# Kernel optimization log

Measured on AMD Instinct MI355X. Metric: run time of the kernel, lower is better.

## Reference

```python
import jax, jax.numpy as jnp
import numpy as np

N = 30000      # num nodes
E = 600000     # num edges
D = 128        # feature dim (all layers)
R = 7          # num_relation
G = 16         # num graphs in batch
L = 3          # num layers (hidden_dims = [128,128,128])


def setup_inputs() -> dict:
    key = jax.random.key(0)
    ks = jax.random.split(key, 10)
    x = jax.random.normal(ks[0], (N, D), dtype=jnp.float32)
    node_in = jax.random.randint(ks[1], (E,), 0, N)
    node_out = jax.random.randint(ks[2], (E,), 0, N)
    relation = jax.random.randint(ks[3], (E,), 0, R)
    edge_weight = jax.random.uniform(ks[4], (E,), dtype=jnp.float32)
    node2graph = jnp.sort(jax.random.randint(ks[5], (N,), 0, G))
    # learned params: per-layer relational linear (R*D -> D) and self-loop linear (D -> D)
    Wr = jax.random.normal(ks[6], (L, R * D, D), dtype=jnp.float32) * 0.02
    br = jnp.zeros((L, D), dtype=jnp.float32)
    Wl = jax.random.normal(ks[7], (L, D, D), dtype=jnp.float32) * 0.02
    bl = jnp.zeros((L, D), dtype=jnp.float32)
    return dict(x=x, node_in=node_in, node_out=node_out, relation=relation,
                edge_weight=edge_weight, node2graph=node2graph,
                Wr=Wr, br=br, Wl=Wl, bl=bl)


def reference(x, node_in, node_out, relation, edge_weight, node2graph, Wr, br, Wl, bl):
    # relation-indexed destination segment: node_out * R + relation
    seg = node_out * R + relation            # (E,)
    ew = edge_weight[:, None]                # (E, 1)
    h = x
    for i in range(L):
        msg = h[node_in] * ew                                         # gather + weight, (E, D)
        upd = jax.ops.segment_sum(msg, seg, num_segments=N * R)       # scatter_add, (N*R, D)
        upd = upd.reshape(N, R * D)                                   # per-relation concat
        h = jax.nn.relu(upd @ Wr[i] + br[i] + h @ Wl[i] + bl[i])      # linear + self-loop + act
    node_feature = h                                                  # (N, D)
    graph_feature = jax.ops.segment_sum(node_feature, node2graph, num_segments=G)  # sum readout
    return graph_feature, node_feature
```

## Files before the change

kernel.cpp:

```cpp
#include <hip/hip_runtime.h>
#include <hip/hip_bf16.h>

#define NN 30000
#define NE 600000
#define DD 128
#define RR 7
#define GG 16
#define LL 3

#define NB64 ((NN + 63) / 64)

typedef short bf16x8 __attribute__((ext_vector_type(8)));
typedef float f32x4  __attribute__((ext_vector_type(4)));

__device__ __forceinline__ unsigned short f2bf(float f) {
    unsigned u = __float_as_uint(f);
    unsigned r = (u + 0x7fffu + ((u >> 16) & 1u)) >> 16;
    return (unsigned short)r;
}
__device__ __forceinline__ float bf2f(unsigned short b) {
    return __uint_as_float(((unsigned)b) << 16);
}
__device__ __forceinline__ ushort2 pk2bf(float a, float b) {
    __hip_bfloat162 t = __float22bfloat162_rn(make_float2(a, b));
    return *(ushort2*)&t;
}

__device__ __forceinline__ void gl_lds16(const void* g, void* l) {
    __builtin_amdgcn_global_load_lds(
        (const __attribute__((address_space(1))) void*)g,
        (__attribute__((address_space(3))) void*)l, 16, 0, 0);
}

__global__ __launch_bounds__(256) void pack_weights(
    const float* __restrict__ Wl,
    const float* __restrict__ Wr,
    unsigned short* __restrict__ Bw2)
{
    int t = blockIdx.x * 256 + threadIdx.x;
    if (t >= LL * 131072) return;
    int l    = t >> 17;
    int rem  = t & 131071;
    int ch   = rem >> 14;
    int c    = (rem >> 7) & 127;
    int kkin = rem & 127;
    float v;
    if (ch == 0) {
        v = Wl[(size_t)l * 16384 + kkin * 128 + c];
    } else {
        v = Wr[(size_t)l * 114688 + (size_t)((ch - 1) * 128 + kkin) * 128 + c];
    }
    Bw2[t] = f2bf(v);
}

__global__ __launch_bounds__(256) void convert_bf16(
    const float* __restrict__ in, unsigned short* __restrict__ out, int n4)
{
    int i = blockIdx.x * 256 + threadIdx.x;
    if (i >= n4) return;
    float4 v = ((const float4*)in)[i];
    ushort2 lo = pk2bf(v.x, v.y);
    ushort2 hi = pk2bf(v.z, v.w);
    ((ushort4*)out)[i] = make_ushort4(lo.x, lo.y, hi.x, hi.y);
}

__global__ __launch_bounds__(256) void bucket_hist(
    const int* __restrict__ node_out, int* __restrict__ bcnt, int E)
{
    int e = blockIdx.x * 256 + threadIdx.x;
    if (e < E) atomicAdd(&bcnt[(node_out[e] >> 6) * 16], 1);
}

__global__ __launch_bounds__(512) void bucket_scan(
    const int* __restrict__ bcnt, int* __restrict__ bstart,
    int* __restrict__ bcur, int nb)
{
    __shared__ int s[512];
    int t = threadIdx.x;
    int v = (t < nb) ? bcnt[t * 16] : 0;
    s[t] = v;
    __syncthreads();
#pragma unroll
    for (int off = 1; off < 512; off <<= 1) {
        int u = (t >= off) ? s[t - off] : 0;
        __syncthreads();
        s[t] += u;
        __syncthreads();
    }
    if (t <= nb) {
        int excl = s[t] - v;
        bstart[t] = excl;
        if (t < nb) bcur[t * 16] = excl;
    }
}

__global__ __launch_bounds__(256) void bucket_scatter(
    const int* __restrict__ node_in,
    const int* __restrict__ node_out,
    const int* __restrict__ relation,
    const float* __restrict__ ew,
    int* __restrict__ bcur,
    int2* __restrict__ tmp,
    int E)
{
    int e = blockIdx.x * 256 + threadIdx.x;
    if (e >= E) return;
    int o = node_out[e];
    int pos = atomicAdd(&bcur[(o >> 6) * 16], 1);
    tmp[pos] = make_int2(((o & 63) << 18) | (node_in[e] << 3) | relation[e],
                         __float_as_int(ew[e]));
}

__global__ __launch_bounds__(256) void bucket_sort(
    const int2* __restrict__ tmp,
    const int* __restrict__ bstart,
    int2* __restrict__ meta,
    int* __restrict__ start,
    int N)
{
    __shared__ int hist[64];
    __shared__ int scan[64];
    __shared__ int cur[64];
    const int b = blockIdx.x;
    const int t = threadIdx.x;
    const int s0 = bstart[b];
    const int s1 = bstart[b + 1];

    if (t < 64) hist[t] = 0;
    __syncthreads();
    for (int i = s0 + t; i < s1; i += 256)
        atomicAdd(&hist[((unsigned)tmp[i].x) >> 18], 1);
    __syncthreads();

    int v = (t < 64) ? hist[t] : 0;
    if (t < 64) scan[t] = v;
    __syncthreads();
#pragma unroll
    for (int off = 1; off < 64; off <<= 1) {
        int u = (t < 64 && t >= off) ? scan[t - off] : 0;
        __syncthreads();
        if (t < 64) scan[t] += u;
        __syncthreads();
    }
    if (t < 64) {
        int excl = scan[t] - v;
        cur[t] = s0 + excl;
        int node = b * 64 + t;
        if (node <= N) start[node] = s0 + excl;
    }
    __syncthreads();

    for (int i = s0 + t; i < s1; i += 256) {
        int2 m = tmp[i];
        int j = ((unsigned)m.x) >> 18;
        int pos = atomicAdd(&cur[j], 1);
        meta[pos] = make_int2(m.x & 0x3ffff, m.y);
    }
}

__global__ __launch_bounds__(256) void aggregate_h(
    const unsigned short* __restrict__ hb,
    const int* __restrict__ start,
    const int2* __restrict__ meta,
    unsigned short* __restrict__ upd,
    int N)
{
    int wid = (blockIdx.x * 256 + threadIdx.x) >> 6;
    int lane = threadIdx.x & 63;
    if (wid >= N) return;

    int e0 = start[wid];
    int e1 = start[wid + 1];

    float ax[7], ay[7];
#pragma unroll
    for (int r = 0; r < 7; ++r) { ax[r] = 0.f; ay[r] = 0.f; }

#define GATHER(m) (*(const unsigned*)(hb + (((size_t)((m).x >> 3)) << 7) + lane * 2))
#define ACCUM(m, u) do {                                                       \
    float w_  = __int_as_float((m).y);                                         \
    float hx_ = __uint_as_float((u) << 16);                                    \
    float hy_ = __uint_as_float((u) & 0xffff0000u);                            \
    switch (__builtin_amdgcn_readfirstlane((m).x) & 7) {                       \
      case 0: ax[0]=fmaf(w_,hx_,ax[0]); ay[0]=fmaf(w_,hy_,ay[0]); break;       \
      case 1: ax[1]=fmaf(w_,hx_,ax[1]); ay[1]=fmaf(w_,hy_,ay[1]); break;       \
      case 2: ax[2]=fmaf(w_,hx_,ax[2]); ay[2]=fmaf(w_,hy_,ay[2]); break;       \
      case 3: ax[3]=fmaf(w_,hx_,ax[3]); ay[3]=fmaf(w_,hy_,ay[3]); break;       \
      case 4: ax[4]=fmaf(w_,hx_,ax[4]); ay[4]=fmaf(w_,hy_,ay[4]); break;       \
      case 5: ax[5]=fmaf(w_,hx_,ax[5]); ay[5]=fmaf(w_,hy_,ay[5]); break;       \
      default: ax[6]=fmaf(w_,hx_,ax[6]); ay[6]=fmaf(w_,hy_,ay[6]); break;      \
    } } while (0)

    int e = e0;
    for (; e + 4 <= e1; e += 4) {
        int2 m0 = meta[e + 0], m1 = meta[e + 1];
        int2 m2 = meta[e + 2], m3 = meta[e + 3];
        unsigned u0 = GATHER(m0), u1 = GATHER(m1);
        unsigned u2 = GATHER(m2), u3 = GATHER(m3);
        ACCUM(m0, u0); ACCUM(m1, u1); ACCUM(m2, u2); ACCUM(m3, u3);
    }
    for (; e < e1; ++e) {
        int2 m = meta[e];
        unsigned u = GATHER(m);
        ACCUM(m, u);
    }
#undef GATHER
#undef ACCUM

    unsigned short* urow = upd + (size_t)wid * 896 + lane * 2;
#pragma unroll
    for (int r = 0; r < 7; ++r) {
        ushort2 p = pk2bf(ax[r], ay[r]);
        *(unsigned*)(urow + r * 128) = ((unsigned)p.y << 16) | p.x;
    }
}

__global__ __launch_bounds__(256) void gemm_fused(
    const unsigned short* __restrict__ hb,
    const unsigned short* __restrict__ upd,
    const unsigned short* __restrict__ Bw2,
    const float* __restrict__ br,
    const float* __restrict__ bl,
    unsigned short* __restrict__ hout,
    float* __restrict__ nf,
    int N)
{
    __shared__ unsigned short As[64 * 128];
    __shared__ unsigned short Bs[128 * 128];

    const int tid  = threadIdx.x;
    const int wave = tid >> 6;
    const int lane = tid & 63;
    const int quad = lane >> 4;
    const int l16  = lane & 15;
    const int row0 = blockIdx.x * 64;

    const int lr = lane >> 4;
    const int ls = lane & 15;

    f32x4 acc[4][2];
#pragma unroll
    for (int mt = 0; mt < 4; ++mt)
#pragma unroll
        for (int nt = 0; nt < 2; ++nt)
            acc[mt][nt] = (f32x4){0.f, 0.f, 0.f, 0.f};

    const unsigned short* As_l = As + l16 * 128;
    const unsigned short* Bs_l = Bs + (wave * 32 + l16) * 128;
    const int swz = l16 & 7;

    for (int ch = 0; ch < 8; ++ch) {
#pragma unroll
        for (int i = 0; i < 4; ++i) {
            int g = i * 4 + wave;
            int r = g * 4 + lr;
            int slot = ls ^ (r & 7);
            const unsigned short* src;
            if (ch == 0)
                src = hb + (size_t)(row0 + r) * 128 + slot * 8;
            else
                src = upd + (size_t)(row0 + r) * 896 + (ch - 1) * 128 + slot * 8;
            gl_lds16(src, As + g * 512);
        }
        const unsigned short* Bchunk = Bw2 + (size_t)ch * 16384;
#pragma unroll
        for (int i = 0; i < 8; ++i) {
            int g = i * 4 + wave;
            int r = g * 4 + lr;
            int slot = ls ^ (r & 7);
            gl_lds16(Bchunk + (size_t)r * 128 + slot * 8, Bs + g * 512);
        }
        __syncthreads();

#pragma unroll
        for (int kc = 0; kc < 4; ++kc) {
            int so = ((kc * 4 + quad) ^ swz) * 8;
            bf16x8 a0 = *(const bf16x8*)(As_l + 0 * 16 * 128 + so);
            bf16x8 a1 = *(const bf16x8*)(As_l + 1 * 16 * 128 + so);
            bf16x8 a2 = *(const bf16x8*)(As_l + 2 * 16 * 128 + so);
            bf16x8 a3 = *(const bf16x8*)(As_l + 3 * 16 * 128 + so);
            bf16x8 b0 = *(const bf16x8*)(Bs_l + 0 * 16 * 128 + so);
            bf16x8 b1 = *(const bf16x8*)(Bs_l + 1 * 16 * 128 + so);
            acc[0][0] = __builtin_amdgcn_mfma_f32_16x16x32_bf16(a0, b0, acc[0][0], 0, 0, 0);
            acc[1][0] = __builtin_amdgcn_mfma_f32_16x16x32_bf16(a1, b0, acc[1][0], 0, 0, 0);
            acc[2][0] = __builtin_amdgcn_mfma_f32_16x16x32_bf16(a2, b0, acc[2][0], 0, 0, 0);
            acc[3][0] = __builtin_amdgcn_mfma_f32_16x16x32_bf16(a3, b0, acc[3][0], 0, 0, 0);
            acc[0][1] = __builtin_amdgcn_mfma_f32_16x16x32_bf16(a0, b1, acc[0][1], 0, 0, 0);
            acc[1][1] = __builtin_amdgcn_mfma_f32_16x16x32_bf16(a1, b1, acc[1][1], 0, 0, 0);
            acc[2][1] = __builtin_amdgcn_mfma_f32_16x16x32_bf16(a2, b1, acc[2][1], 0, 0, 0);
            acc[3][1] = __builtin_amdgcn_mfma_f32_16x16x32_bf16(a3, b1, acc[3][1], 0, 0, 0);
        }
        __syncthreads();
    }

    const int ncol = wave * 32 + l16;
    float bias0 = br[ncol] + bl[ncol];
    float bias1 = br[ncol + 16] + bl[ncol + 16];
#pragma unroll
    for (int mt = 0; mt < 4; ++mt) {
#pragma unroll
        for (int reg = 0; reg < 4; ++reg) {
            int row = row0 + mt * 16 + quad * 4 + reg;
            if (row < N) {
                float v0 = fmaxf(acc[mt][0][reg] + bias0, 0.f);
                float v1 = fmaxf(acc[mt][1][reg] + bias1, 0.f);
                if (hout) {
                    ushort2 p = pk2bf(v0, v1);
                    hout[(size_t)row * DD + ncol]      = p.x;
                    hout[(size_t)row * DD + ncol + 16] = p.y;
                }
                if (nf) {
                    nf[(size_t)row * DD + ncol]      = v0;
                    nf[(size_t)row * DD + ncol + 16] = v1;
                }
            }
        }
    }
}

__global__ __launch_bounds__(256) void graph_sum(
    const float* __restrict__ nf,
    const int* __restrict__ n2g,
    float* __restrict__ gf,
    int N)
{
    int t = blockIdx.x * 256 + threadIdx.x;
    int chunk = t >> 5;
    int lane = t & 31;
    int n0 = chunk * 16;
    if (n0 >= N) return;
    int nend = n0 + 16; if (nend > N) nend = N;

    float4 acc = make_float4(0.f, 0.f, 0.f, 0.f);
    int curg = n2g[n0];
    for (int n = n0; n < nend; ++n) {
        int g = n2g[n];
        if (g != curg) {
            float* dst = gf + (size_t)curg * DD + lane * 4;
            atomicAdd(dst + 0, acc.x); atomicAdd(dst + 1, acc.y);
            atomicAdd(dst + 2, acc.z); atomicAdd(dst + 3, acc.w);
            acc = make_float4(0.f, 0.f, 0.f, 0.f);
            curg = g;
        }
        float4 v = *(const float4*)(nf + (size_t)n * DD + lane * 4);
        acc.x += v.x; acc.y += v.y; acc.z += v.z; acc.w += v.w;
    }
    float* dst = gf + (size_t)curg * DD + lane * 4;
    atomicAdd(dst + 0, acc.x); atomicAdd(dst + 1, acc.y);
    atomicAdd(dst + 2, acc.z); atomicAdd(dst + 3, acc.w);
}

extern "C" void kernel_launch(void* const* d_in, const int* in_sizes, int n_in,
                              void* d_out, int out_size, void* d_ws, size_t ws_size,
                              hipStream_t stream)
{
    const float* x        = (const float*)d_in[0];
    const int*   node_in  = (const int*)d_in[1];
    const int*   node_out = (const int*)d_in[2];
    const int*   relation = (const int*)d_in[3];
    const float* ew       = (const float*)d_in[4];
    const int*   n2g      = (const int*)d_in[5];
    const float* Wr       = (const float*)d_in[6];
    const float* br       = (const float*)d_in[7];
    const float* Wl       = (const float*)d_in[8];
    const float* bl       = (const float*)d_in[9];

    float* out = (float*)d_out;
    float* gf = out;
    float* nf = out + GG * DD;

    char* w = (char*)d_ws;
    unsigned short* upd  = (unsigned short*)w; w += (size_t)NN * RR * DD * 2;
    unsigned short* hbA  = (unsigned short*)w; w += (size_t)NN * DD * 2;
    unsigned short* hbB  = (unsigned short*)w; w += (size_t)NN * DD * 2;
    unsigned short* Bw2  = (unsigned short*)w; w += (size_t)LL * 131072 * 2;
    int2*  meta   = (int2*)w;                  w += (size_t)NE * 8;
    int2*  tmp    = (int2*)w;                  w += (size_t)NE * 8;
    int*   start  = (int*)w;                   w += (size_t)(NN + 1) * 4 + 60;
    int*   bcnt   = (int*)w;                   w += (size_t)NB64 * 16 * 4 + 64;
    int*   bcur   = (int*)w;                   w += (size_t)NB64 * 16 * 4 + 64;
    int*   bstart = (int*)w;                   w += (size_t)(NB64 + 1) * 4 + 60;

    const int N = NN, E = NE;

    pack_weights<<<(LL * 131072 + 255) / 256, 256, 0, stream>>>(Wl, Wr, Bw2);
    convert_bf16<<<(N * DD / 4 + 255) / 256, 256, 0, stream>>>(x, hbA, N * DD / 4);

    hipMemsetAsync(bcnt, 0, (size_t)NB64 * 16 * sizeof(int), stream);
    bucket_hist<<<(E + 255) / 256, 256, 0, stream>>>(node_out, bcnt, E);
    bucket_scan<<<1, 512, 0, stream>>>(bcnt, bstart, bcur, NB64);
    bucket_scatter<<<(E + 255) / 256, 256, 0, stream>>>(
        node_in, node_out, relation, ew, bcur, tmp, E);
    bucket_sort<<<NB64, 256, 0, stream>>>(tmp, bstart, meta, start, N);

    unsigned short* hin = hbA;
    unsigned short* hnext = hbB;
    for (int l = 0; l < LL; ++l) {
        const float* br_l = br + (size_t)l * DD;
        const float* bl_l = bl + (size_t)l * DD;
        const unsigned short* Bw2_l = Bw2 + (size_t)l * 131072;
        bool last = (l == LL - 1);

        aggregate_h<<<(N * 64 + 255) / 256, 256, 0, stream>>>(
            hin, start, meta, upd, N);

        gemm_fused<<<(N + 63) / 64, 256, 0, stream>>>(
            hin, upd, Bw2_l, br_l, bl_l,
            last ? (unsigned short*)nullptr : hnext,
            last ? nf : (float*)nullptr, N);

        unsigned short* t = hin; hin = hnext; hnext = t;
    }

    hipMemsetAsync(gf, 0, (size_t)GG * DD * sizeof(float), stream);
    int chunks = (N + 15) / 16;
    graph_sum<<<(chunks * 32 + 255) / 256, 256, 0, stream>>>(nf, n2g, gf, N);
}
```

Measured before the change: 358.1 us.

## Store relation aggregates as fp8, widen gather to 16B per lane, fuse prologue

The per-relation aggregate buffer is now stored in fp8 instead of bf16, which halves its write and read traffic between the aggregation and GEMM kernels. The GEMM converts it back to bf16 while staging into LDS. Aggregation now has each 16-lane group handle a separate edge with 16-byte gathers, then combines the groups with cross-lane shuffles. To make this work, node features and weights are stored in a permuted column order. Weight packing, x conversion and the two memsets are merged into one prologue kernel, at the cost of fp8 precision loss in the aggregates.

```diff
diff --git a/kernel.cpp b/kernel.cpp
--- a/kernel.cpp
+++ b/kernel.cpp
@@ -10,58 +10,74 @@
 
 #define NB64 ((NN + 63) / 64)
 
+#define NPK (LL * 8 * 128 * 32)
+#define NCV (NN * 32)
+
 typedef short bf16x8 __attribute__((ext_vector_type(8)));
 typedef float f32x4  __attribute__((ext_vector_type(4)));
+typedef float f32x2  __attribute__((ext_vector_type(2)));
+
 
 __device__ __forceinline__ unsigned short f2bf(float f) {
     unsigned u = __float_as_uint(f);
     unsigned r = (u + 0x7fffu + ((u >> 16) & 1u)) >> 16;
     return (unsigned short)r;
 }
-__device__ __forceinline__ float bf2f(unsigned short b) {
-    return __uint_as_float(((unsigned)b) << 16);
-}
 __device__ __forceinline__ ushort2 pk2bf(float a, float b) {
     __hip_bfloat162 t = __float22bfloat162_rn(make_float2(a, b));
     return *(ushort2*)&t;
 }
-
 __device__ __forceinline__ void gl_lds16(const void* g, void* l) {
     __builtin_amdgcn_global_load_lds(
         (const __attribute__((address_space(1))) void*)g,
         (__attribute__((address_space(3))) void*)l, 16, 0, 0);
 }
 
-__global__ __launch_bounds__(256) void pack_weights(
+__global__ __launch_bounds__(256) void prologue(
     const float* __restrict__ Wl,
     const float* __restrict__ Wr,
-    unsigned short* __restrict__ Bw2)
+    unsigned short* __restrict__ Bw16,
+    const float* __restrict__ x,
+    unsigned short* __restrict__ hb,
+    int* __restrict__ bcnt,
+    float* __restrict__ gf)
 {
     int t = blockIdx.x * 256 + threadIdx.x;
-    if (t >= LL * 131072) return;
-    int l    = t >> 17;
-    int rem  = t & 131071;
-    int ch   = rem >> 14;
-    int c    = (rem >> 7) & 127;
-    int kkin = rem & 127;
-    float v;
-    if (ch == 0) {
-        v = Wl[(size_t)l * 16384 + kkin * 128 + c];
+    if (t < NPK) {
+        int k4 = t & 31;
+        int n  = (t >> 5) & 127;
+        int ch = (t >> 12) & 7;
+        int l  = t >> 15;
+        unsigned short o[4];
+#pragma unroll
+        for (int j = 0; j < 4; ++j) {
+            int k_pos = k4 * 4 + j;
+            int kp = k_pos & 63;
+            int k = (k_pos & ~63) + (kp & 3) * 16 + (kp >> 2);
+            float w = (ch == 0)
+                ? Wl[(size_t)l * 16384 + k * 128 + n]
+                : Wr[(size_t)l * 114688 + (size_t)((ch - 1) * 128 + k) * 128 + n];
+            o[j] = f2bf(w);
+        }
+        ((ushort4*)Bw16)[t] = make_ushort4(o[0], o[1], o[2], o[3]);
+    } else if (t < NPK + NCV) {
+        int i = t - NPK;
+        int row = i >> 5;
+        int pg  = i & 31;
+        int span = pg >> 4;
+        int q = pg & 15;
+        const float* xr = x + (size_t)row * DD + span * 64 + q;
+        ushort2 a = pk2bf(xr[0],  xr[16]);
+        ushort2 b = pk2bf(xr[32], xr[48]);
+        ((ushort4*)hb)[i] = make_ushort4(a.x, a.y, b.x, b.y);
     } else {
-        v = Wr[(size_t)l * 114688 + (size_t)((ch - 1) * 128 + kkin) * 128 + c];
-    }
-    Bw2[t] = f2bf(v);
-}
-
-__global__ __launch_bounds__(256) void convert_bf16(
-    const float* __restrict__ in, unsigned short* __restrict__ out, int n4)
-{
-    int i = blockIdx.x * 256 + threadIdx.x;
-    if (i >= n4) return;
-    float4 v = ((const float4*)in)[i];
-    ushort2 lo = pk2bf(v.x, v.y);
-    ushort2 hi = pk2bf(v.z, v.w);
-    ((ushort4*)out)[i] = make_ushort4(lo.x, lo.y, hi.x, hi.y);
+        int i = t - NPK - NCV;
+        if (i < NB64 * 16) bcnt[i] = 0;
+        else {
+            i -= NB64 * 16;
+            if (i < GG * DD) gf[i] = 0.f;
+        }
+    }
 }
 
 __global__ __launch_bounds__(256) void bucket_hist(
@@ -154,7 +170,9 @@
         int2 m = tmp[i];
         int j = ((unsigned)m.x) >> 18;
         int pos = atomicAdd(&cur[j], 1);
-        meta[pos] = make_int2(m.x & 0x3ffff, m.y);
+        int key = m.x & 0x3ffff;
+        int in = key >> 3, rel = key & 7;
+        meta[pos] = make_int2((in << 8) | rel, m.y);
     }
 }
 
@@ -162,63 +180,105 @@
     const unsigned short* __restrict__ hb,
     const int* __restrict__ start,
     const int2* __restrict__ meta,
-    unsigned short* __restrict__ upd,
+    unsigned char* __restrict__ upd,
     int N)
 {
     int wid = (blockIdx.x * 256 + threadIdx.x) >> 6;
     int lane = threadIdx.x & 63;
     if (wid >= N) return;
 
+    const int grp  = lane >> 4;
+    const int l16  = lane & 15;
+    const int base = l16 * 16;
+    const char* hB = (const char*)hb;
+
     int e0 = start[wid];
     int e1 = start[wid + 1];
 
-    float ax[7], ay[7];
-#pragma unroll
-    for (int r = 0; r < 7; ++r) { ax[r] = 0.f; ay[r] = 0.f; }
-
-#define GATHER(m) (*(const unsigned*)(hb + (((size_t)((m).x >> 3)) << 7) + lane * 2))
-#define ACCUM(m, u) do {                                                       \
-    float w_  = __int_as_float((m).y);                                         \
-    float hx_ = __uint_as_float((u) << 16);                                    \
-    float hy_ = __uint_as_float((u) & 0xffff0000u);                            \
-    switch (__builtin_amdgcn_readfirstlane((m).x) & 7) {                       \
-      case 0: ax[0]=fmaf(w_,hx_,ax[0]); ay[0]=fmaf(w_,hy_,ay[0]); break;       \
-      case 1: ax[1]=fmaf(w_,hx_,ax[1]); ay[1]=fmaf(w_,hy_,ay[1]); break;       \
-      case 2: ax[2]=fmaf(w_,hx_,ax[2]); ay[2]=fmaf(w_,hy_,ay[2]); break;       \
-      case 3: ax[3]=fmaf(w_,hx_,ax[3]); ay[3]=fmaf(w_,hy_,ay[3]); break;       \
-      case 4: ax[4]=fmaf(w_,hx_,ax[4]); ay[4]=fmaf(w_,hy_,ay[4]); break;       \
-      case 5: ax[5]=fmaf(w_,hx_,ax[5]); ay[5]=fmaf(w_,hy_,ay[5]); break;       \
-      default: ax[6]=fmaf(w_,hx_,ax[6]); ay[6]=fmaf(w_,hy_,ay[6]); break;      \
-    } } while (0)
+    float acc[7][8];
+#pragma unroll
+    for (int r = 0; r < 7; ++r)
+#pragma unroll
+        for (int j = 0; j < 8; ++j) acc[r][j] = 0.f;
+
+#define FMA_CASE(R)                                     \
+    acc[R][0] = fmaf(wt, d0, acc[R][0]);                \
+    acc[R][1] = fmaf(wt, d1, acc[R][1]);                \
+    acc[R][2] = fmaf(wt, d2, acc[R][2]);                \
+    acc[R][3] = fmaf(wt, d3, acc[R][3]);                \
+    acc[R][4] = fmaf(wt, d4, acc[R][4]);                \
+    acc[R][5] = fmaf(wt, d5, acc[R][5]);                \
+    acc[R][6] = fmaf(wt, d6, acc[R][6]);                \
+    acc[R][7] = fmaf(wt, d7, acc[R][7]);
+
+#define PROC_EDGE(m, u) do {                                            \
+    float wt = __int_as_float((m).y);                                   \
+    float d0 = __uint_as_float((u).x << 16);                            \
+    float d1 = __uint_as_float((u).x & 0xffff0000u);                    \
+    float d2 = __uint_as_float((u).y << 16);                            \
+    float d3 = __uint_as_float((u).y & 0xffff0000u);                    \
+    float d4 = __uint_as_float((u).z << 16);                            \
+    float d5 = __uint_as_float((u).z & 0xffff0000u);                    \
+    float d6 = __uint_as_float((u).w << 16);                            \
+    float d7 = __uint_as_float((u).w & 0xffff0000u);                    \
+    switch ((m).x & 7) {                                                \
+        case 0: FMA_CASE(0) break;                                      \
+        case 1: FMA_CASE(1) break;                                      \
+        case 2: FMA_CASE(2) break;                                      \
+        case 3: FMA_CASE(3) break;                                      \
+        case 4: FMA_CASE(4) break;                                      \
+        case 5: FMA_CASE(5) break;                                      \
+        default: FMA_CASE(6) break;                                     \
+    }                                                                   \
+} while (0)
 
     int e = e0;
+    for (; e + 8 <= e1; e += 8) {
+        int2 m0 = meta[e + grp];
+        int2 m1 = meta[e + 4 + grp];
+        uint4 u0 = *(const uint4*)(hB + ((unsigned)m0.x & 0xffffff00u) + base);
+        uint4 u1 = *(const uint4*)(hB + ((unsigned)m1.x & 0xffffff00u) + base);
+        PROC_EDGE(m0, u0);
+        PROC_EDGE(m1, u1);
+    }
     for (; e + 4 <= e1; e += 4) {
-        int2 m0 = meta[e + 0], m1 = meta[e + 1];
-        int2 m2 = meta[e + 2], m3 = meta[e + 3];
-        unsigned u0 = GATHER(m0), u1 = GATHER(m1);
-        unsigned u2 = GATHER(m2), u3 = GATHER(m3);
-        ACCUM(m0, u0); ACCUM(m1, u1); ACCUM(m2, u2); ACCUM(m3, u3);
-    }
-    for (; e < e1; ++e) {
-        int2 m = meta[e];
-        unsigned u = GATHER(m);
-        ACCUM(m, u);
-    }
-#undef GATHER
-#undef ACCUM
-
-    unsigned short* urow = upd + (size_t)wid * 896 + lane * 2;
-#pragma unroll
-    for (int r = 0; r < 7; ++r) {
-        ushort2 p = pk2bf(ax[r], ay[r]);
-        *(unsigned*)(urow + r * 128) = ((unsigned)p.y << 16) | p.x;
-    }
-}
-
-__global__ __launch_bounds__(256) void gemm_fused(
+        int2 m = meta[e + grp];
+        uint4 u = *(const uint4*)(hB + ((unsigned)m.x & 0xffffff00u) + base);
+        PROC_EDGE(m, u);
+    }
+    if (e + grp < e1) {
+        int2 m = meta[e + grp];
+        uint4 u = *(const uint4*)(hB + ((unsigned)m.x & 0xffffff00u) + base);
+        PROC_EDGE(m, u);
+    }
+#undef PROC_EDGE
+#undef FMA_CASE
+
+#pragma unroll
+    for (int r = 0; r < 7; ++r)
+#pragma unroll
+        for (int j = 0; j < 8; ++j) {
+            acc[r][j] += __shfl_xor(acc[r][j], 16, 64);
+            acc[r][j] += __shfl_xor(acc[r][j], 32, 64);
+        }
+
+    if (grp == 0) {
+        unsigned char* dst = upd + (size_t)wid * 896 + l16 * 8;
+#pragma unroll
+        for (int r = 0; r < 7; ++r) {
+            int lo = __builtin_amdgcn_cvt_pk_fp8_f32(acc[r][0], acc[r][1], 0, false);
+            lo = __builtin_amdgcn_cvt_pk_fp8_f32(acc[r][2], acc[r][3], lo, true);
+            int hi = __builtin_amdgcn_cvt_pk_fp8_f32(acc[r][4], acc[r][5], 0, false);
+            hi = __builtin_amdgcn_cvt_pk_fp8_f32(acc[r][6], acc[r][7], hi, true);
+            *(uint2*)(dst + r * 128) = make_uint2((unsigned)lo, (unsigned)hi);
+        }
+    }
+}
+
+__global__ __launch_bounds__(256) void gemm_h(
     const unsigned short* __restrict__ hb,
-    const unsigned short* __restrict__ upd,
-    const unsigned short* __restrict__ Bw2,
+    const unsigned char* __restrict__ upd,
+    const unsigned short* __restrict__ Bw16,
     const float* __restrict__ br,
     const float* __restrict__ bl,
     unsigned short* __restrict__ hout,
@@ -234,7 +294,6 @@
     const int quad = lane >> 4;
     const int l16  = lane & 15;
     const int row0 = blockIdx.x * 64;
-
     const int lr = lane >> 4;
     const int ls = lane & 15;
 
@@ -250,52 +309,66 @@
     const int swz = l16 & 7;
 
     for (int ch = 0; ch < 8; ++ch) {
-#pragma unroll
-        for (int i = 0; i < 4; ++i) {
-            int g = i * 4 + wave;
-            int r = g * 4 + lr;
-            int slot = ls ^ (r & 7);
-            const unsigned short* src;
-            if (ch == 0)
-                src = hb + (size_t)(row0 + r) * 128 + slot * 8;
-            else
-                src = upd + (size_t)(row0 + r) * 896 + (ch - 1) * 128 + slot * 8;
-            gl_lds16(src, As + g * 512);
-        }
-        const unsigned short* Bchunk = Bw2 + (size_t)ch * 16384;
+        if (ch == 0) {
+#pragma unroll
+            for (int i = 0; i < 4; ++i) {
+                int g = i * 4 + wave;
+                int r = g * 4 + lr;
+                int slot = ls ^ (r & 7);
+                gl_lds16(hb + (size_t)(row0 + r) * 128 + slot * 8, As + g * 512);
+            }
+        } else {
+            const unsigned char* usrc = upd + (size_t)row0 * 896 + (ch - 1) * 128;
+#pragma unroll
+            for (int i = 0; i < 4; ++i) {
+                int sid = i * 256 + tid;
+                int r = sid >> 4, s = sid & 15;
+                uint2 u = *(const uint2*)(usrc + (size_t)r * 896 + s * 8);
+                f32x2 c0 = __builtin_amdgcn_cvt_pk_f32_fp8(u.x, false);
+                f32x2 c1 = __builtin_amdgcn_cvt_pk_f32_fp8(u.x, true);
+                f32x2 c2 = __builtin_amdgcn_cvt_pk_f32_fp8(u.y, false);
+                f32x2 c3 = __builtin_amdgcn_cvt_pk_f32_fp8(u.y, true);
+                ushort2 p0 = pk2bf(c0[0], c0[1]);
+                ushort2 p1 = pk2bf(c1[0], c1[1]);
+                ushort2 p2 = pk2bf(c2[0], c2[1]);
+                ushort2 p3 = pk2bf(c3[0], c3[1]);
+                uint4 o;
+                o.x = (unsigned)p0.x | ((unsigned)p0.y << 16);
+                o.y = (unsigned)p1.x | ((unsigned)p1.y << 16);
+                o.z = (unsigned)p2.x | ((unsigned)p2.y << 16);
+                o.w = (unsigned)p3.x | ((unsigned)p3.y << 16);
+                ((uint4*)As)[r * 16 + (s ^ (r & 7))] = o;
+            }
+        }
+        const unsigned short* Bsrc = Bw16 + (size_t)ch * 16384;
 #pragma unroll
         for (int i = 0; i < 8; ++i) {
             int g = i * 4 + wave;
             int r = g * 4 + lr;
             int slot = ls ^ (r & 7);
-            gl_lds16(Bchunk + (size_t)r * 128 + slot * 8, Bs + g * 512);
+            gl_lds16(Bsrc + (size_t)r * 128 + slot * 8, Bs + g * 512);
         }
         __syncthreads();
 
 #pragma unroll
         for (int kc = 0; kc < 4; ++kc) {
             int so = ((kc * 4 + quad) ^ swz) * 8;
-            bf16x8 a0 = *(const bf16x8*)(As_l + 0 * 16 * 128 + so);
-            bf16x8 a1 = *(const bf16x8*)(As_l + 1 * 16 * 128 + so);
-            bf16x8 a2 = *(const bf16x8*)(As_l + 2 * 16 * 128 + so);
-            bf16x8 a3 = *(const bf16x8*)(As_l + 3 * 16 * 128 + so);
-            bf16x8 b0 = *(const bf16x8*)(Bs_l + 0 * 16 * 128 + so);
-            bf16x8 b1 = *(const bf16x8*)(Bs_l + 1 * 16 * 128 + so);
-            acc[0][0] = __builtin_amdgcn_mfma_f32_16x16x32_bf16(a0, b0, acc[0][0], 0, 0, 0);
-            acc[1][0] = __builtin_amdgcn_mfma_f32_16x16x32_bf16(a1, b0, acc[1][0], 0, 0, 0);
-            acc[2][0] = __builtin_amdgcn_mfma_f32_16x16x32_bf16(a2, b0, acc[2][0], 0, 0, 0);
-            acc[3][0] = __builtin_amdgcn_mfma_f32_16x16x32_bf16(a3, b0, acc[3][0], 0, 0, 0);
-            acc[0][1] = __builtin_amdgcn_mfma_f32_16x16x32_bf16(a0, b1, acc[0][1], 0, 0, 0);
-            acc[1][1] = __builtin_amdgcn_mfma_f32_16x16x32_bf16(a1, b1, acc[1][1], 0, 0, 0);
-            acc[2][1] = __builtin_amdgcn_mfma_f32_16x16x32_bf16(a2, b1, acc[2][1], 0, 0, 0);
-            acc[3][1] = __builtin_amdgcn_mfma_f32_16x16x32_bf16(a3, b1, acc[3][1], 0, 0, 0);
-        }
-        __syncthreads();
-    }
-
-    const int ncol = wave * 32 + l16;
-    float bias0 = br[ncol] + bl[ncol];
-    float bias1 = br[ncol + 16] + bl[ncol + 16];
+            bf16x8 b0 = *(const bf16x8*)(Bs_l + so);
+            bf16x8 b1 = *(const bf16x8*)(Bs_l + 16 * 128 + so);
+#pragma unroll
+            for (int mt = 0; mt < 4; ++mt) {
+                bf16x8 a = *(const bf16x8*)(As_l + mt * 16 * 128 + so);
+                acc[mt][0] = __builtin_amdgcn_mfma_f32_16x16x32_bf16(a, b0, acc[mt][0], 0, 0, 0);
+                acc[mt][1] = __builtin_amdgcn_mfma_f32_16x16x32_bf16(a, b1, acc[mt][1], 0, 0, 0);
+            }
+        }
+        __syncthreads();
+    }
+
+    const int c0 = wave * 32 + l16;
+    const float bias0 = br[c0] + bl[c0];
+    const float bias1 = br[c0 + 16] + bl[c0 + 16];
+    const int pbase = (wave >> 1) * 64 + l16 * 4 + (wave & 1) * 2;
 #pragma unroll
     for (int mt = 0; mt < 4; ++mt) {
 #pragma unroll
@@ -306,12 +379,11 @@
                 float v1 = fmaxf(acc[mt][1][reg] + bias1, 0.f);
                 if (hout) {
                     ushort2 p = pk2bf(v0, v1);
-                    hout[(size_t)row * DD + ncol]      = p.x;
-                    hout[(size_t)row * DD + ncol + 16] = p.y;
+                    *(ushort2*)(hout + (size_t)row * 128 + pbase) = p;
                 }
                 if (nf) {
-                    nf[(size_t)row * DD + ncol]      = v0;
-                    nf[(size_t)row * DD + ncol + 16] = v1;
+                    nf[(size_t)row * DD + c0]      = v0;
+                    nf[(size_t)row * DD + c0 + 16] = v1;
                 }
             }
         }
@@ -370,10 +442,10 @@
     float* nf = out + GG * DD;
 
     char* w = (char*)d_ws;
-    unsigned short* upd  = (unsigned short*)w; w += (size_t)NN * RR * DD * 2;
+    unsigned char*  upd  = (unsigned char*)w;  w += (size_t)NN * RR * DD;
     unsigned short* hbA  = (unsigned short*)w; w += (size_t)NN * DD * 2;
     unsigned short* hbB  = (unsigned short*)w; w += (size_t)NN * DD * 2;
-    unsigned short* Bw2  = (unsigned short*)w; w += (size_t)LL * 131072 * 2;
+    unsigned short* Bw16 = (unsigned short*)w; w += (size_t)LL * 8 * 128 * 128 * 2;
     int2*  meta   = (int2*)w;                  w += (size_t)NE * 8;
     int2*  tmp    = (int2*)w;                  w += (size_t)NE * 8;
     int*   start  = (int*)w;                   w += (size_t)(NN + 1) * 4 + 60;
@@ -383,10 +455,10 @@
 
     const int N = NN, E = NE;
 
-    pack_weights<<<(LL * 131072 + 255) / 256, 256, 0, stream>>>(Wl, Wr, Bw2);
-    convert_bf16<<<(N * DD / 4 + 255) / 256, 256, 0, stream>>>(x, hbA, N * DD / 4);
-
-    hipMemsetAsync(bcnt, 0, (size_t)NB64 * 16 * sizeof(int), stream);
+    int ptot = NPK + NCV + NB64 * 16 + GG * DD;
+    prologue<<<(ptot + 255) / 256, 256, 0, stream>>>(
+        Wl, Wr, Bw16, x, hbA, bcnt, gf);
+
     bucket_hist<<<(E + 255) / 256, 256, 0, stream>>>(node_out, bcnt, E);
     bucket_scan<<<1, 512, 0, stream>>>(bcnt, bstart, bcur, NB64);
     bucket_scatter<<<(E + 255) / 256, 256, 0, stream>>>(
@@ -398,21 +470,20 @@
     for (int l = 0; l < LL; ++l) {
         const float* br_l = br + (size_t)l * DD;
         const float* bl_l = bl + (size_t)l * DD;
-        const unsigned short* Bw2_l = Bw2 + (size_t)l * 131072;
+        const unsigned short* Bw_l = Bw16 + (size_t)l * 8 * 128 * 128;
         bool last = (l == LL - 1);
 
         aggregate_h<<<(N * 64 + 255) / 256, 256, 0, stream>>>(
             hin, start, meta, upd, N);
 
-        gemm_fused<<<(N + 63) / 64, 256, 0, stream>>>(
-            hin, upd, Bw2_l, br_l, bl_l,
+        gemm_h<<<(N + 63) / 64, 256, 0, stream>>>(
+            hin, upd, Bw_l, br_l, bl_l,
             last ? (unsigned short*)nullptr : hnext,
             last ? nf : (float*)nullptr, N);
 
         unsigned short* t = hin; hin = hnext; hnext = t;
     }
 
-    hipMemsetAsync(gf, 0, (size_t)GG * DD * sizeof(float), stream);
     int chunks = (N + 15) / 16;
     graph_sum<<<(chunks * 32 + 255) / 256, 256, 0, stream>>>(nf, n2g, gf, N);
 }
```

Result: slower. 383.7 us (+7.1%).
